# Kernel tuning notes

Measured on AMD Instinct MI355X. Metric: run time of the kernel, lower is better.

Reference implementation:

```python
import jax, jax.numpy as jnp
import numpy as np
import math

N_QUBITS = 8
N_LAYERS = 2
EMBED = 512
HEADS = 64
B, T = 2, 1024


def _ry(state, theta, wire, off):
    # state: (batch?, 2, 2, ..., 2); theta: scalar or (N,)
    ax = off + wire
    st = jnp.moveaxis(state, ax, -1)
    s0, s1 = st[..., 0], st[..., 1]
    half = jnp.asarray(theta) * 0.5
    c, s = jnp.cos(half), jnp.sin(half)
    if c.ndim:  # batched angles -> broadcast over remaining qubit axes
        c = c.reshape((-1,) + (1,) * (s0.ndim - 1))
        s = s.reshape((-1,) + (1,) * (s0.ndim - 1))
    new = jnp.stack([c * s0 - s * s1, s * s0 + c * s1], axis=-1)
    return jnp.moveaxis(new, -1, ax)


def _cnot(state, cw, tw, off):
    st = jnp.moveaxis(state, (off + cw, off + tw), (-2, -1))
    new = jnp.stack([st[..., 0, :], st[..., 1, ::-1]], axis=-2)
    return jnp.moveaxis(new, (-2, -1), (off + cw, off + tw))


def _entangling_state(params):
    # Fixed-parameter block applied to |0...0>: single shared statevector.
    n = N_QUBITS
    psi = jnp.zeros((2,) * n, dtype=params.dtype).at[(0,) * n].set(1.0)
    for l in range(N_LAYERS):
        for q in range(n):
            psi = _ry(psi, params[l, q], q, 0)
        for q in range(n - 1):
            psi = _cnot(psi, q, q + 1, 0)
        psi = _cnot(psi, n - 1, 0, 0)
    return psi


def _quantum_heads(angles, params):
    # angles: (N, n_qubits) data-encoding RY angles; returns (N, n_qubits) <Z_q>.
    n = N_QUBITS
    psi0 = _entangling_state(params)
    state = jnp.broadcast_to(psi0, (angles.shape[0],) + (2,) * n)
    for q in range(n):
        state = _ry(state, angles[:, q], q, 1)
    probs = state * state  # real statevector -> probabilities
    zs = []
    for q in range(n):
        axes = tuple(a for a in range(1, n + 1) if a != q + 1)
        m = probs.sum(axes)  # (N, 2)
        zs.append(m[:, 0] - m[:, 1])
    return jnp.stack(zs, axis=-1)


def setup_inputs() -> dict:
    key = jax.random.key(0)
    kx, kq, kk, kv, kp = jax.random.split(key, 5)
    scale = 1.0 / math.sqrt(EMBED)
    return {
        "x": jax.random.normal(kx, (B, T, EMBED), dtype=jnp.float32),
        "Wq": jax.random.normal(kq, (EMBED, EMBED), dtype=jnp.float32) * scale,
        "Wk": jax.random.normal(kk, (EMBED, EMBED), dtype=jnp.float32) * scale,
        "Wv": jax.random.normal(kv, (EMBED, EMBED), dtype=jnp.float32) * scale,
        "params": jax.random.normal(kp, (N_LAYERS, N_QUBITS), dtype=jnp.float32),
    }


def reference(x, Wq, Wk, Wv, params):
    Bx, Tx, E = x.shape
    head_dim = E // HEADS
    q = x @ Wq.T
    k = x @ Wk.T
    v = x @ Wv.T
    # NOTE: attention on the full embed dim (no head split), scaled by sqrt(E).
    scores = jnp.einsum("bte,bse->bts", q, k) / jnp.sqrt(jnp.asarray(E, x.dtype))
    weights = jax.nn.softmax(scores, axis=-1)
    out = jnp.einsum("bts,bse->bte", weights, v)
    heads = out.reshape(Bx, Tx, HEADS, head_dim)[..., :N_QUBITS]
    angles = heads.reshape(-1, N_QUBITS)  # (B*T*HEADS, n_qubits)
    z = _quantum_heads(angles, params)
    return z.reshape(Bx, Tx, HEADS * N_QUBITS)
```

## Files before the change

kernel.cpp:

```cpp
#include <hip/hip_runtime.h>
#include <math.h>

typedef __attribute__((ext_vector_type(8))) short bf16x8;
typedef __attribute__((ext_vector_type(4))) float f32x4;

__device__ __forceinline__ ushort f2b(float f) {
    unsigned u = __float_as_uint(f);
    return (ushort)((u + 0x7FFFu + ((u >> 16) & 1u)) >> 16);
}

__device__ __forceinline__ void gl16(const ushort* g, ushort* l) {
    __builtin_amdgcn_global_load_lds((const __attribute__((address_space(1))) void*)g,
                                     (__attribute__((address_space(3))) void*)l, 16, 0, 0);
}

__device__ __forceinline__ void stage128(const ushort* g, int ld, ushort* lds,
                                         int w, int lane) {
    const int rsub = lane >> 3;
    const size_t coff = (size_t)(((lane & 7) ^ (rsub & 7)) * 8);
#pragma unroll
    for (int ii = 0; ii < 4; ++ii) {
        const int i = w * 4 + ii;
        gl16(g + (size_t)(i * 8 + rsub) * ld + coff, lds + i * 512);
    }
}
__device__ __forceinline__ void stage64(const ushort* g, int ld, ushort* lds,
                                        int w, int lane) {
    const int rsub = lane >> 3;
    const size_t coff = (size_t)(((lane & 7) ^ (rsub & 7)) * 8);
#pragma unroll
    for (int ii = 0; ii < 2; ++ii) {
        const int i = w * 2 + ii;
        gl16(g + (size_t)(i * 8 + rsub) * ld + coff, lds + i * 512);
    }
}

__device__ __forceinline__ bf16x8 frag(const ushort* lds, int row0, int c, int lane) {
    const int r = row0 + (lane & 15);
    const int slot = (c * 4 + (lane >> 4)) ^ (r & 7);
    return *(const bf16x8*)(lds + (size_t)r * 64 + slot * 8);
}

__device__ __forceinline__ void compute128(const ushort* As, const ushort* Bs,
                                           f32x4 acc[4][4], int lane, int wr, int wc) {
#pragma unroll
    for (int c = 0; c < 2; ++c) {
        bf16x8 a[4], b[4];
#pragma unroll
        for (int f = 0; f < 4; ++f) {
            a[f] = frag(As, wr * 64 + f * 16, c, lane);
            b[f] = frag(Bs, wc * 64 + f * 16, c, lane);
        }
#pragma unroll
        for (int i = 0; i < 4; ++i)
#pragma unroll
            for (int j = 0; j < 4; ++j)
                acc[i][j] = __builtin_amdgcn_mfma_f32_16x16x32_bf16(a[i], b[j], acc[i][j], 0, 0, 0);
    }
}

__device__ __forceinline__ void compute64(const ushort* As, const ushort* Bs,
                                          f32x4 acc[2][2], int lane, int wr, int wc) {
#pragma unroll
    for (int c = 0; c < 2; ++c) {
        bf16x8 a[2], b[2];
#pragma unroll
        for (int f = 0; f < 2; ++f) {
            a[f] = frag(As, wr * 32 + f * 16, c, lane);
            b[f] = frag(Bs, wc * 32 + f * 16, c, lane);
        }
#pragma unroll
        for (int i = 0; i < 2; ++i)
#pragma unroll
            for (int j = 0; j < 2; ++j)
                acc[i][j] = __builtin_amdgcn_mfma_f32_16x16x32_bf16(a[i], b[j], acc[i][j], 0, 0, 0);
    }
}

__global__ __launch_bounds__(256) void cvtq_kernel(const float* __restrict__ x,
                                                   const float* __restrict__ wq,
                                                   const float* __restrict__ wk,
                                                   const float* __restrict__ wv,
                                                   const float* __restrict__ params,
                                                   ushort* __restrict__ xb,
                                                   ushort* __restrict__ wqb,
                                                   ushort* __restrict__ wkb,
                                                   ushort* __restrict__ wvb,
                                                   float* __restrict__ ab) {
    const int tid = threadIdx.x;
    if (blockIdx.y < 4) {
        const int z = blockIdx.y;
        const float* src = (z == 0) ? x : (z == 1) ? wq : (z == 2) ? wk : wv;
        ushort* dst = (z == 0) ? xb : (z == 1) ? wqb : (z == 2) ? wkb : wvb;
        const int n = (z == 0) ? (2048 * 512) : (512 * 512);
        const int i = (blockIdx.x * 256 + tid) * 8;
        if (i >= n) return;
        float4 v0 = *(const float4*)(src + i);
        float4 v1 = *(const float4*)(src + i + 4);
        ushort t[8] = {f2b(v0.x), f2b(v0.y), f2b(v0.z), f2b(v0.w),
                       f2b(v1.x), f2b(v1.y), f2b(v1.z), f2b(v1.w)};
        *(uint4*)(dst + i) = *(uint4*)t;
        return;
    }
    if (blockIdx.x != 0) return;
    __shared__ float st[256];
    __shared__ float red[64];
    st[tid] = (tid == 0) ? 1.0f : 0.0f;
    __syncthreads();
    for (int l = 0; l < 2; ++l) {
        for (int q = 0; q < 8; ++q) {
            float h = 0.5f * params[l * 8 + q];
            float c = cosf(h), s = sinf(h);
            int str = 1 << (7 - q);
            if ((tid & str) == 0) {
                float s0 = st[tid], s1 = st[tid + str];
                st[tid]       = c * s0 - s * s1;
                st[tid + str] = s * s0 + c * s1;
            }
            __syncthreads();
        }
        for (int q = 0; q < 8; ++q) {
            int cw = q, tw = (q + 1) & 7;
            int cs = 1 << (7 - cw), ts = 1 << (7 - tw);
            if ((tid & cs) && !(tid & ts)) {
                float a = st[tid], b = st[tid ^ ts];
                st[tid] = b;
                st[tid ^ ts] = a;
            }
            __syncthreads();
        }
    }
    const float amp = st[tid];
    float v[16];
#pragma unroll
    for (int q = 0; q < 8; ++q) {
        int str = 1 << (7 - q);
        v[q]     = amp * amp * ((tid & str) ? -1.0f : 1.0f);
        v[8 + q] = ((tid & str) == 0) ? 2.0f * amp * st[tid ^ str] : 0.0f;
    }
#pragma unroll
    for (int off = 32; off; off >>= 1)
#pragma unroll
        for (int q = 0; q < 16; ++q) v[q] += __shfl_xor(v[q], off);
    const int lane = tid & 63, wid = tid >> 6;
    if (lane == 0)
#pragma unroll
        for (int q = 0; q < 16; ++q) red[wid * 16 + q] = v[q];
    __syncthreads();
    if (tid < 16) ab[tid] = red[tid] + red[16 + tid] + red[32 + tid] + red[48 + tid];
}

__global__ __launch_bounds__(256) void qkv_mfma(const ushort* __restrict__ xb,
                                                const ushort* __restrict__ wqb,
                                                const ushort* __restrict__ wkb,
                                                const ushort* __restrict__ wvb,
                                                ushort* __restrict__ qb,
                                                ushort* __restrict__ kb,
                                                ushort* __restrict__ vT) {
    __shared__ ushort As[2][128 * 64];
    __shared__ ushort Bs[2][128 * 64];
    const int tid = threadIdx.x, lane = tid & 63, w = tid >> 6;
    const int wr = w >> 1, wc = w & 1;
    const int z = blockIdx.z;
    int m0, n0, ldc;
    const ushort *A, *B;
    ushort* C;
    if (z < 2) {
        m0 = blockIdx.x << 7;  n0 = blockIdx.y << 7;
        A = xb;  B = (z == 0) ? wqb : wkb;  C = (z == 0) ? qb : kb;  ldc = 512;
    } else {
        m0 = blockIdx.y << 7;  n0 = blockIdx.x << 7;
        A = wvb;  B = xb;  C = vT;  ldc = 2048;
    }
    const ushort* Ap = A + (size_t)m0 * 512;
    const ushort* Bp = B + (size_t)n0 * 512;
    stage128(Ap, 512, As[0], w, lane);
    stage128(Bp, 512, Bs[0], w, lane);
    __syncthreads();
    f32x4 acc[4][4] = {};
    for (int t = 0; t < 8; ++t) {
        const int cur = t & 1;
        if (t < 7) {
            stage128(Ap + (t + 1) * 64, 512, As[cur ^ 1], w, lane);
            stage128(Bp + (t + 1) * 64, 512, Bs[cur ^ 1], w, lane);
        }
        compute128(As[cur], Bs[cur], acc, lane, wr, wc);
        __syncthreads();
    }
    const int rb2 = (lane >> 4) << 2, cc = lane & 15;
#pragma unroll
    for (int fr = 0; fr < 4; ++fr)
#pragma unroll
        for (int fc = 0; fc < 4; ++fc) {
            int row = m0 + wr * 64 + fr * 16 + rb2;
            int col = n0 + wc * 64 + fc * 16 + cc;
#pragma unroll
            for (int r = 0; r < 4; ++r)
                C[(size_t)(row + r) * ldc + col] = f2b(acc[fr][fc][r]);
        }
}

__global__ __launch_bounds__(256) void scores_mfma(const ushort* __restrict__ qb,
                                                   const ushort* __restrict__ kb,
                                                   float* __restrict__ sb) {
    __shared__ ushort As[2][64 * 64];
    __shared__ ushort Bs[2][64 * 64];
    const int tid = threadIdx.x, lane = tid & 63, w = tid >> 6;
    const int wr = w >> 1, wc = w & 1;
    const int m0 = blockIdx.x << 6, n0 = blockIdx.y << 6, z = blockIdx.z;
    const ushort* Ap = qb + (size_t)z * 1024 * 512 + (size_t)m0 * 512;
    const ushort* Bp = kb + (size_t)z * 1024 * 512 + (size_t)n0 * 512;
    float* C = sb + (size_t)z * 1024 * 1024;
    stage64(Ap, 512, As[0], w, lane);
    stage64(Bp, 512, Bs[0], w, lane);
    __syncthreads();
    f32x4 acc[2][2] = {};
    for (int t = 0; t < 8; ++t) {
        const int cur = t & 1;
        if (t < 7) {
            stage64(Ap + (t + 1) * 64, 512, As[cur ^ 1], w, lane);
            stage64(Bp + (t + 1) * 64, 512, Bs[cur ^ 1], w, lane);
        }
        compute64(As[cur], Bs[cur], acc, lane, wr, wc);
        __syncthreads();
    }
    const float scale = 0.044194173824159216f;
    const int rb2 = (lane >> 4) << 2, cc = lane & 15;
#pragma unroll
    for (int fr = 0; fr < 2; ++fr)
#pragma unroll
        for (int fc = 0; fc < 2; ++fc) {
            int row = m0 + wr * 32 + fr * 16 + rb2;
            int col = n0 + wc * 32 + fc * 16 + cc;
#pragma unroll
            for (int r = 0; r < 4; ++r)
                C[(size_t)(row + r) * 1024 + col] = acc[fr][fc][r] * scale;
        }
}

__global__ __launch_bounds__(256) void softmax_kernel(const float* __restrict__ S,
                                                      ushort* __restrict__ W) {
    const int row = blockIdx.x, tid = threadIdx.x;
    const float* p = S + (size_t)row * 1024;
    float4 v = ((const float4*)p)[tid];
    float m = fmaxf(fmaxf(v.x, v.y), fmaxf(v.z, v.w));
#pragma unroll
    for (int off = 32; off; off >>= 1) m = fmaxf(m, __shfl_xor(m, off));
    __shared__ float sm[4];
    __shared__ float ss[4];
    const int wid = tid >> 6, lane = tid & 63;
    if (lane == 0) sm[wid] = m;
    __syncthreads();
    m = fmaxf(fmaxf(sm[0], sm[1]), fmaxf(sm[2], sm[3]));
    float e0 = expf(v.x - m), e1 = expf(v.y - m), e2 = expf(v.z - m), e3 = expf(v.w - m);
    float s = e0 + e1 + e2 + e3;
#pragma unroll
    for (int off = 32; off; off >>= 1) s += __shfl_xor(s, off);
    if (lane == 0) ss[wid] = s;
    __syncthreads();
    s = ss[0] + ss[1] + ss[2] + ss[3];
    float r = 1.0f / s;
    ushort4 o = {f2b(e0 * r), f2b(e1 * r), f2b(e2 * r), f2b(e3 * r)};
    ((ushort4*)(W + (size_t)row * 1024))[tid] = o;
}

__global__ __launch_bounds__(256) void pv_mfma(const ushort* __restrict__ wb,
                                               const ushort* __restrict__ vT,
                                               float* __restrict__ out,
                                               const float* __restrict__ ab) {
    __shared__ ushort As[2][64 * 64];
    __shared__ ushort Bs[2][64 * 64];
    const int tid = threadIdx.x, lane = tid & 63, w = tid >> 6;
    const int wr = w >> 1, wc = w & 1;
    const int m0 = blockIdx.x << 6, n0 = blockIdx.y << 6, z = blockIdx.z;
    const ushort* Ap = wb + (size_t)z * 1024 * 1024 + (size_t)m0 * 1024;
    const ushort* Bp = vT + (size_t)n0 * 2048 + z * 1024;
    float* C = out + (size_t)z * 1024 * 512;
    stage64(Ap, 1024, As[0], w, lane);
    stage64(Bp, 2048, Bs[0], w, lane);
    __syncthreads();
    f32x4 acc[2][2] = {};
    for (int t = 0; t < 16; ++t) {
        const int cur = t & 1;
        if (t < 15) {
            stage64(Ap + (t + 1) * 64, 1024, As[cur ^ 1], w, lane);
            stage64(Bp + (t + 1) * 64, 2048, Bs[cur ^ 1], w, lane);
        }
        compute64(As[cur], Bs[cur], acc, lane, wr, wc);
        __syncthreads();
    }
    const float Aq = ab[lane & 7], Bq = ab[8 + (lane & 7)];
    const int rb2 = (lane >> 4) << 2, cc = lane & 15;
#pragma unroll
    for (int fr = 0; fr < 2; ++fr)
#pragma unroll
        for (int fc = 0; fc < 2; ++fc) {
            int row = m0 + wr * 32 + fr * 16 + rb2;
            int col = n0 + wc * 32 + fc * 16 + cc;
#pragma unroll
            for (int r = 0; r < 4; ++r) {
                float sn, cs;
                sincosf(acc[fr][fc][r], &sn, &cs);
                C[(size_t)(row + r) * 512 + col] = cs * Aq - sn * Bq;
            }
        }
}

extern "C" void kernel_launch(void* const* d_in, const int* in_sizes, int n_in,
                              void* d_out, int out_size, void* d_ws, size_t ws_size,
                              hipStream_t stream) {
    const float* x      = (const float*)d_in[0];
    const float* Wq     = (const float*)d_in[1];
    const float* Wk     = (const float*)d_in[2];
    const float* Wv     = (const float*)d_in[3];
    const float* params = (const float*)d_in[4];
    float* out = (float*)d_out;

    char* base = (char*)d_ws;
    float*  ab  = (float*)base;
    ushort* xb  = (ushort*)(base + 256);
    ushort* wqb = xb + 2048 * 512;
    ushort* wkb = wqb + 512 * 512;
    ushort* wvb = wkb + 512 * 512;
    ushort* qb  = wvb + 512 * 512;
    ushort* kb  = qb + 2048 * 512;
    ushort* vT  = kb + 2048 * 512;
    float*  sb  = (float*)(vT + 2048 * 512);
    ushort* wb  = (ushort*)(sb + 2 * 1024 * 1024);

    hipLaunchKernelGGL(cvtq_kernel, dim3(512, 5), dim3(256), 0, stream,
                       x, Wq, Wk, Wv, params, xb, wqb, wkb, wvb, ab);
    hipLaunchKernelGGL(qkv_mfma, dim3(16, 4, 3), dim3(256), 0, stream,
                       xb, wqb, wkb, wvb, qb, kb, vT);
    hipLaunchKernelGGL(scores_mfma, dim3(16, 16, 2), dim3(256), 0, stream, qb, kb, sb);
    hipLaunchKernelGGL(softmax_kernel, dim3(2048), dim3(256), 0, stream, sb, wb);
    hipLaunchKernelGGL(pv_mfma, dim3(16, 8, 2), dim3(256), 0, stream, wb, vT, out, ab);
}
```

Before: 111.3 us.

## Triple-buffer GEMM LDS pipeline and shrink QKV tiles to 64x64

All three MFMA GEMM kernels move from double-buffered LDS staging with full __syncthreads to a three-stage ring buffer. Each kernel prefetches two K-tiles ahead and uses an explicit s_waitcnt vmcnt(4) plus s_barrier, so global loads stay in flight across iterations. The QKV projection also switches from 128x128 tiles to 64x64 tiles with four times as many blocks, which improves occupancy and CU fill for the small problem at the cost of less operand reuse per block. The hand-written waitcnt depends on the exact number of outstanding loads per wave, which is fragile if the compiler reorders them.

New measurement: 97.74 us. 1.14x faster.

```diff
diff --git a/kernel.cpp b/kernel.cpp
--- a/kernel.cpp
+++ b/kernel.cpp
@@ -14,16 +14,9 @@
                                      (__attribute__((address_space(3))) void*)l, 16, 0, 0);
 }
 
-__device__ __forceinline__ void stage128(const ushort* g, int ld, ushort* lds,
-                                         int w, int lane) {
-    const int rsub = lane >> 3;
-    const size_t coff = (size_t)(((lane & 7) ^ (rsub & 7)) * 8);
-#pragma unroll
-    for (int ii = 0; ii < 4; ++ii) {
-        const int i = w * 4 + ii;
-        gl16(g + (size_t)(i * 8 + rsub) * ld + coff, lds + i * 512);
-    }
-}
+__device__ __forceinline__ void wait_pipe() { asm volatile("s_waitcnt vmcnt(4) lgkmcnt(0)" ::: "memory"); }
+__device__ __forceinline__ void wait_all()  { asm volatile("s_waitcnt vmcnt(0) lgkmcnt(0)" ::: "memory"); }
+
 __device__ __forceinline__ void stage64(const ushort* g, int ld, ushort* lds,
                                         int w, int lane) {
     const int rsub = lane >> 3;
@@ -39,24 +32,6 @@
     const int r = row0 + (lane & 15);
     const int slot = (c * 4 + (lane >> 4)) ^ (r & 7);
     return *(const bf16x8*)(lds + (size_t)r * 64 + slot * 8);
-}
-
-__device__ __forceinline__ void compute128(const ushort* As, const ushort* Bs,
-                                           f32x4 acc[4][4], int lane, int wr, int wc) {
-#pragma unroll
-    for (int c = 0; c < 2; ++c) {
-        bf16x8 a[4], b[4];
-#pragma unroll
-        for (int f = 0; f < 4; ++f) {
-            a[f] = frag(As, wr * 64 + f * 16, c, lane);
-            b[f] = frag(Bs, wc * 64 + f * 16, c, lane);
-        }
-#pragma unroll
-        for (int i = 0; i < 4; ++i)
-#pragma unroll
-            for (int j = 0; j < 4; ++j)
-                acc[i][j] = __builtin_amdgcn_mfma_f32_16x16x32_bf16(a[i], b[j], acc[i][j], 0, 0, 0);
-    }
 }
 
 __device__ __forceinline__ void compute64(const ushort* As, const ushort* Bs,
@@ -157,8 +132,7 @@
                                                 ushort* __restrict__ qb,
                                                 ushort* __restrict__ kb,
                                                 ushort* __restrict__ vT) {
-    __shared__ ushort As[2][128 * 64];
-    __shared__ ushort Bs[2][128 * 64];
+    __shared__ ushort lds[3][2 * 64 * 64];
     const int tid = threadIdx.x, lane = tid & 63, w = tid >> 6;
     const int wr = w >> 1, wc = w & 1;
     const int z = blockIdx.z;
@@ -166,34 +140,39 @@
     const ushort *A, *B;
     ushort* C;
     if (z < 2) {
-        m0 = blockIdx.x << 7;  n0 = blockIdx.y << 7;
+        m0 = blockIdx.x << 6;  n0 = blockIdx.y << 6;
         A = xb;  B = (z == 0) ? wqb : wkb;  C = (z == 0) ? qb : kb;  ldc = 512;
     } else {
-        m0 = blockIdx.y << 7;  n0 = blockIdx.x << 7;
+        m0 = blockIdx.y << 6;  n0 = blockIdx.x << 6;
         A = wvb;  B = xb;  C = vT;  ldc = 2048;
     }
     const ushort* Ap = A + (size_t)m0 * 512;
     const ushort* Bp = B + (size_t)n0 * 512;
-    stage128(Ap, 512, As[0], w, lane);
-    stage128(Bp, 512, Bs[0], w, lane);
-    __syncthreads();
-    f32x4 acc[4][4] = {};
-    for (int t = 0; t < 8; ++t) {
-        const int cur = t & 1;
-        if (t < 7) {
-            stage128(Ap + (t + 1) * 64, 512, As[cur ^ 1], w, lane);
-            stage128(Bp + (t + 1) * 64, 512, Bs[cur ^ 1], w, lane);
-        }
-        compute128(As[cur], Bs[cur], acc, lane, wr, wc);
-        __syncthreads();
+    stage64(Ap, 512, lds[0], w, lane);
+    stage64(Bp, 512, lds[0] + 4096, w, lane);
+    stage64(Ap + 64, 512, lds[1], w, lane);
+    stage64(Bp + 64, 512, lds[1] + 4096, w, lane);
+    f32x4 acc[2][2] = {};
+    const int NT = 8;
+    for (int t = 0; t < NT; ++t) {
+        if (t < NT - 1) wait_pipe(); else wait_all();
+        __builtin_amdgcn_s_barrier();
+        __builtin_amdgcn_sched_barrier(0);
+        if (t + 2 < NT) {
+            ushort* nb = lds[(t + 2) % 3];
+            stage64(Ap + (t + 2) * 64, 512, nb, w, lane);
+            stage64(Bp + (t + 2) * 64, 512, nb + 4096, w, lane);
+        }
+        const ushort* cb = lds[t % 3];
+        compute64(cb, cb + 4096, acc, lane, wr, wc);
     }
     const int rb2 = (lane >> 4) << 2, cc = lane & 15;
 #pragma unroll
-    for (int fr = 0; fr < 4; ++fr)
-#pragma unroll
-        for (int fc = 0; fc < 4; ++fc) {
-            int row = m0 + wr * 64 + fr * 16 + rb2;
-            int col = n0 + wc * 64 + fc * 16 + cc;
+    for (int fr = 0; fr < 2; ++fr)
+#pragma unroll
+        for (int fc = 0; fc < 2; ++fc) {
+            int row = m0 + wr * 32 + fr * 16 + rb2;
+            int col = n0 + wc * 32 + fc * 16 + cc;
 #pragma unroll
             for (int r = 0; r < 4; ++r)
                 C[(size_t)(row + r) * ldc + col] = f2b(acc[fr][fc][r]);
@@ -203,26 +182,30 @@
 __global__ __launch_bounds__(256) void scores_mfma(const ushort* __restrict__ qb,
                                                    const ushort* __restrict__ kb,
                                                    float* __restrict__ sb) {
-    __shared__ ushort As[2][64 * 64];
-    __shared__ ushort Bs[2][64 * 64];
+    __shared__ ushort lds[3][2 * 64 * 64];
     const int tid = threadIdx.x, lane = tid & 63, w = tid >> 6;
     const int wr = w >> 1, wc = w & 1;
     const int m0 = blockIdx.x << 6, n0 = blockIdx.y << 6, z = blockIdx.z;
     const ushort* Ap = qb + (size_t)z * 1024 * 512 + (size_t)m0 * 512;
     const ushort* Bp = kb + (size_t)z * 1024 * 512 + (size_t)n0 * 512;
     float* C = sb + (size_t)z * 1024 * 1024;
-    stage64(Ap, 512, As[0], w, lane);
-    stage64(Bp, 512, Bs[0], w, lane);
-    __syncthreads();
+    stage64(Ap, 512, lds[0], w, lane);
+    stage64(Bp, 512, lds[0] + 4096, w, lane);
+    stage64(Ap + 64, 512, lds[1], w, lane);
+    stage64(Bp + 64, 512, lds[1] + 4096, w, lane);
     f32x4 acc[2][2] = {};
-    for (int t = 0; t < 8; ++t) {
-        const int cur = t & 1;
-        if (t < 7) {
-            stage64(Ap + (t + 1) * 64, 512, As[cur ^ 1], w, lane);
-            stage64(Bp + (t + 1) * 64, 512, Bs[cur ^ 1], w, lane);
-        }
-        compute64(As[cur], Bs[cur], acc, lane, wr, wc);
-        __syncthreads();
+    const int NT = 8;
+    for (int t = 0; t < NT; ++t) {
+        if (t < NT - 1) wait_pipe(); else wait_all();
+        __builtin_amdgcn_s_barrier();
+        __builtin_amdgcn_sched_barrier(0);
+        if (t + 2 < NT) {
+            ushort* nb = lds[(t + 2) % 3];
+            stage64(Ap + (t + 2) * 64, 512, nb, w, lane);
+            stage64(Bp + (t + 2) * 64, 512, nb + 4096, w, lane);
+        }
+        const ushort* cb = lds[t % 3];
+        compute64(cb, cb + 4096, acc, lane, wr, wc);
     }
     const float scale = 0.044194173824159216f;
     const int rb2 = (lane >> 4) << 2, cc = lane & 15;
@@ -268,26 +251,30 @@
                                                const ushort* __restrict__ vT,
                                                float* __restrict__ out,
                                                const float* __restrict__ ab) {
-    __shared__ ushort As[2][64 * 64];
-    __shared__ ushort Bs[2][64 * 64];
+    __shared__ ushort lds[3][2 * 64 * 64];
     const int tid = threadIdx.x, lane = tid & 63, w = tid >> 6;
     const int wr = w >> 1, wc = w & 1;
     const int m0 = blockIdx.x << 6, n0 = blockIdx.y << 6, z = blockIdx.z;
     const ushort* Ap = wb + (size_t)z * 1024 * 1024 + (size_t)m0 * 1024;
     const ushort* Bp = vT + (size_t)n0 * 2048 + z * 1024;
     float* C = out + (size_t)z * 1024 * 512;
-    stage64(Ap, 1024, As[0], w, lane);
-    stage64(Bp, 2048, Bs[0], w, lane);
-    __syncthreads();
+    stage64(Ap, 1024, lds[0], w, lane);
+    stage64(Bp, 2048, lds[0] + 4096, w, lane);
+    stage64(Ap + 64, 1024, lds[1], w, lane);
+    stage64(Bp + 64, 2048, lds[1] + 4096, w, lane);
     f32x4 acc[2][2] = {};
-    for (int t = 0; t < 16; ++t) {
-        const int cur = t & 1;
-        if (t < 15) {
-            stage64(Ap + (t + 1) * 64, 1024, As[cur ^ 1], w, lane);
-            stage64(Bp + (t + 1) * 64, 2048, Bs[cur ^ 1], w, lane);
-        }
-        compute64(As[cur], Bs[cur], acc, lane, wr, wc);
-        __syncthreads();
+    const int NT = 16;
+    for (int t = 0; t < NT; ++t) {
+        if (t < NT - 1) wait_pipe(); else wait_all();
+        __builtin_amdgcn_s_barrier();
+        __builtin_amdgcn_sched_barrier(0);
+        if (t + 2 < NT) {
+            ushort* nb = lds[(t + 2) % 3];
+            stage64(Ap + (t + 2) * 64, 1024, nb, w, lane);
+            stage64(Bp + (t + 2) * 64, 2048, nb + 4096, w, lane);
+        }
+        const ushort* cb = lds[t % 3];
+        compute64(cb, cb + 4096, acc, lane, wr, wc);
     }
     const float Aq = ab[lane & 7], Bq = ab[8 + (lane & 7)];
     const int rb2 = (lane >> 4) << 2, cc = lane & 15;
@@ -330,7 +317,7 @@
 
     hipLaunchKernelGGL(cvtq_kernel, dim3(512, 5), dim3(256), 0, stream,
                        x, Wq, Wk, Wv, params, xb, wqb, wkb, wvb, ab);
-    hipLaunchKernelGGL(qkv_mfma, dim3(16, 4, 3), dim3(256), 0, stream,
+    hipLaunchKernelGGL(qkv_mfma, dim3(32, 8, 3), dim3(256), 0, stream,
                        xb, wqb, wkb, wvb, qb, kb, vT);
     hipLaunchKernelGGL(scores_mfma, dim3(16, 16, 2), dim3(256), 0, stream, qb, kb, sb);
     hipLaunchKernelGGL(softmax_kernel, dim3(2048), dim3(256), 0, stream, sb, wb);
```
